# Optimization experiments

Hardware: AMD Instinct MI355X
Metric: run time of the kernel (lower is better)

## Reference

```python
import jax, jax.numpy as jnp
import numpy as np

N, D, B, M, E, Q, MPT = 100000, 128, 512, 4, 10, 5, 8


def setup_inputs() -> dict:
    key = jax.random.key(0)
    ks = jax.random.split(key, 20)
    return {
        "emb": jax.random.normal(ks[0], (N, D), jnp.float32) * 0.05,
        "delta": jax.random.uniform(ks[1], (N,), jnp.float32, 0.5, 1.5),
        "W": jax.random.normal(ks[2], (D, D), jnp.float32) / D,
        "distance_att": jax.random.normal(ks[3], (E,), jnp.float32),
        "metapath_att": jax.random.normal(ks[4], (MPT,), jnp.float32),
        "s_node": jax.random.randint(ks[5], (B,), 0, N, jnp.int32),
        "t_node": jax.random.randint(ks[6], (B,), 0, N, jnp.int32),
        "s_t_time": jax.random.uniform(ks[7], (B,), jnp.float32, 0.0, 10.0),
        "mp_src": jax.random.randint(ks[8], (B, M, E), 0, N, jnp.int32),
        "mp_dst": jax.random.randint(ks[9], (B, M, E), 0, N, jnp.int32),
        "mp_time": jax.random.uniform(ks[10], (B, M, E), jnp.float32, 0.0, 10.0),
        "mp_dist": jax.random.randint(ks[11], (B, M, E), 0, E, jnp.int32),
        "mp_type": jax.random.randint(ks[12], (B, M), 0, MPT, jnp.int32),
        "neg_node": jax.random.randint(ks[13], (B, Q), 0, N, jnp.int32),
        "neg_mp_src": jax.random.randint(ks[14], (B, Q, M, E), 0, N, jnp.int32),
        "neg_mp_dst": jax.random.randint(ks[15], (B, Q, M, E), 0, N, jnp.int32),
        "neg_mp_time": jax.random.uniform(ks[16], (B, Q, M, E), jnp.float32, 0.0, 10.0),
        "neg_mp_dist": jax.random.randint(ks[17], (B, Q, M, E), 0, E, jnp.int32),
        "neg_mp_type": jax.random.randint(ks[18], (B, Q, M), 0, MPT, jnp.int32),
    }


def reference(emb, delta, W, distance_att, metapath_att,
              s_node, t_node, s_t_time,
              mp_src, mp_dst, mp_time, mp_dist, mp_type,
              neg_node, neg_mp_src, neg_mp_dst, neg_mp_time, neg_mp_dist, neg_mp_type):
    eps = 1e-6

    def sim(ea, eb):
        # bilinear similarity e_a^T W e_b, broadcast over leading dims
        return jnp.sum((ea @ W) * eb, axis=-1)

    dis_att = jax.nn.softmax(distance_att)      # [E]
    mp_att = jax.nn.softmax(metapath_att)       # [MPT]

    d_s = delta[s_node]                          # [B]
    d_t = delta[t_node]                          # [B]

    # ---- positive metapath influence ----
    edge_sim = sim(emb[mp_src], emb[mp_dst])                       # [B,M,E]
    decay = jnp.exp(-(d_s * d_t)[:, None, None]
                    * jnp.abs(s_t_time[:, None, None] - mp_time))  # [B,M,E]
    single_mp = jnp.sum(edge_sim * dis_att[mp_dist] * decay, -1)   # [B,M]
    mp_influ = jnp.sum(single_mp * mp_att[mp_type], -1)            # [B]
    p_lambda = sim(emb[s_node], emb[t_node]) + mp_influ            # [B]

    # ---- negative samples ----
    d_neg = delta[neg_node]                                        # [B,Q]
    n_edge_sim = sim(emb[neg_mp_src], emb[neg_mp_dst])             # [B,Q,M,E]
    n_decay = jnp.exp(-(d_s[:, None] * d_neg)[:, :, None, None]
                      * jnp.abs(s_t_time[:, None, None, None] - neg_mp_time))
    n_single = jnp.sum(n_edge_sim * dis_att[neg_mp_dist] * n_decay, -1)  # [B,Q,M]
    n_influ = jnp.sum(n_single * mp_att[neg_mp_type], -1)          # [B,Q]
    s_neg_sim = sim(emb[s_node][:, None, :], emb[neg_node])        # [B,Q]
    n_lambda = jnp.sum(jnp.log(jax.nn.sigmoid(-(s_neg_sim + n_influ)) + eps), -1)  # [B]

    loss = -jnp.log(jax.nn.sigmoid(p_lambda) + eps) - n_lambda     # [B]
    return loss
```

## Files before the change

kernel.cpp:

```cpp
#include <hip/hip_runtime.h>
#include <hip/hip_bf16.h>
#include <math.h>

constexpr int D   = 128;
constexpr int M   = 4;
constexpr int E   = 10;
constexpr int Q   = 5;
constexpr int MPT = 8;
constexpr int MXE = M * E;
constexpr int TASKS = 1 + MXE + Q + Q * MXE;

__global__ __launch_bounds__(256, 4)
void embw_gemm(const float* __restrict__ emb,
               const float* __restrict__ W,
               float* __restrict__ embW,
               int nrows)
{
    const int jg   = threadIdx.x & 15;
    const int rg   = threadIdx.x >> 4;
    const int base = blockIdx.x * 128;
    int row0 = base + rg * 8;
    if (row0 + 8 > nrows) row0 = nrows - 8;

    const float* ap = emb + (size_t)row0 * D;
    const float* wp = W + jg * 4;

    float acc[8][8];
#pragma unroll
    for (int r = 0; r < 8; ++r)
#pragma unroll
        for (int c = 0; c < 8; ++c) acc[r][c] = 0.f;

    float4 a[8];

#pragma unroll 1
    for (int i0 = 0; i0 < D; i0 += 8) {
#pragma unroll
        for (int r = 0; r < 8; ++r)
            a[r] = *reinterpret_cast<const float4*>(ap + r * D + i0);
#pragma unroll
        for (int u = 0; u < 4; ++u) {
            const float4 wlo = *reinterpret_cast<const float4*>(wp + u * D);
            const float4 whi = *reinterpret_cast<const float4*>(wp + u * D + 64);
#pragma unroll
            for (int r = 0; r < 8; ++r) {
                float e = (u == 0) ? a[r].x : (u == 1) ? a[r].y
                        : (u == 2) ? a[r].z : a[r].w;
                acc[r][0] = fmaf(e, wlo.x, acc[r][0]);
                acc[r][1] = fmaf(e, wlo.y, acc[r][1]);
                acc[r][2] = fmaf(e, wlo.z, acc[r][2]);
                acc[r][3] = fmaf(e, wlo.w, acc[r][3]);
                acc[r][4] = fmaf(e, whi.x, acc[r][4]);
                acc[r][5] = fmaf(e, whi.y, acc[r][5]);
                acc[r][6] = fmaf(e, whi.z, acc[r][6]);
                acc[r][7] = fmaf(e, whi.w, acc[r][7]);
            }
        }

#pragma unroll
        for (int r = 0; r < 8; ++r)
            a[r] = *reinterpret_cast<const float4*>(ap + r * D + i0 + 4);
#pragma unroll
        for (int u = 0; u < 4; ++u) {
            const float4 wlo = *reinterpret_cast<const float4*>(wp + (4 + u) * D);
            const float4 whi = *reinterpret_cast<const float4*>(wp + (4 + u) * D + 64);
#pragma unroll
            for (int r = 0; r < 8; ++r) {
                float e = (u == 0) ? a[r].x : (u == 1) ? a[r].y
                        : (u == 2) ? a[r].z : a[r].w;
                acc[r][0] = fmaf(e, wlo.x, acc[r][0]);
                acc[r][1] = fmaf(e, wlo.y, acc[r][1]);
                acc[r][2] = fmaf(e, wlo.z, acc[r][2]);
                acc[r][3] = fmaf(e, wlo.w, acc[r][3]);
                acc[r][4] = fmaf(e, whi.x, acc[r][4]);
                acc[r][5] = fmaf(e, whi.y, acc[r][5]);
                acc[r][6] = fmaf(e, whi.z, acc[r][6]);
                acc[r][7] = fmaf(e, whi.w, acc[r][7]);
            }
        }

        wp += 8 * D;
    }

#pragma unroll
    for (int r = 0; r < 8; ++r) {
        float* rowp = embW + (size_t)(row0 + r) * D;
        *reinterpret_cast<float4*>(rowp + jg * 4) =
            make_float4(acc[r][0], acc[r][1], acc[r][2], acc[r][3]);
        *reinterpret_cast<float4*>(rowp + 64 + jg * 4) =
            make_float4(acc[r][4], acc[r][5], acc[r][6], acc[r][7]);
    }
}

__device__ __forceinline__ void block_softmaxes(const float* distance_att,
                                                const float* metapath_att,
                                                float* s_dis, float* s_mp,
                                                int tid)
{
    if (tid == 0) {
        float v[E];
        float mx = -1e30f;
        for (int i = 0; i < E; ++i) { v[i] = distance_att[i]; mx = fmaxf(mx, v[i]); }
        float sum = 0.f;
        for (int i = 0; i < E; ++i) { v[i] = expf(v[i] - mx); sum += v[i]; }
        for (int i = 0; i < E; ++i) s_dis[i] = v[i] / sum;

        float w[MPT];
        mx = -1e30f;
        for (int i = 0; i < MPT; ++i) { w[i] = metapath_att[i]; mx = fmaxf(mx, w[i]); }
        sum = 0.f;
        for (int i = 0; i < MPT; ++i) { w[i] = expf(w[i] - mx); sum += w[i]; }
        for (int i = 0; i < MPT; ++i) s_mp[i] = w[i] / sum;
    }
}

__device__ __forceinline__ void decode_task(
    int task, int b, int s, int t, float tt, float dss, float dsdt,
    const float* __restrict__ delta,
    const float* __restrict__ s_dis, const float* __restrict__ s_mp,
    const int* __restrict__ mp_src, const int* __restrict__ mp_dst,
    const float* __restrict__ mp_time, const int* __restrict__ mp_dist,
    const int* __restrict__ mp_type,
    const int* __restrict__ neg_node,
    const int* __restrict__ neg_mp_src, const int* __restrict__ neg_mp_dst,
    const float* __restrict__ neg_mp_time, const int* __restrict__ neg_mp_dist,
    const int* __restrict__ neg_mp_type,
    int& srcn, int& dstn, int& slot, float& wgt)
{
    if (task == 0) {
        srcn = s; dstn = t; slot = 0; wgt = 1.f;
    } else if (task <= MXE) {
        int pe = task - 1;
        int m  = pe / E;
        int idx = b * MXE + pe;
        srcn = mp_src[idx];
        dstn = mp_dst[idx];
        slot = 0;
        float dec = expf(-dsdt * fabsf(tt - mp_time[idx]));
        wgt = s_dis[mp_dist[idx]] * dec * s_mp[mp_type[b * M + m]];
    } else if (task <= MXE + Q) {
        int q = task - 1 - MXE;
        srcn = s;
        dstn = neg_node[b * Q + q];
        slot = 1 + q;
        wgt  = 1.f;
    } else {
        int ne  = task - 1 - MXE - Q;
        int q   = ne / MXE;
        int rem = ne - q * MXE;
        int m   = rem / E;
        int idx = (b * Q + q) * MXE + rem;
        srcn = neg_mp_src[idx];
        dstn = neg_mp_dst[idx];
        slot = 1 + q;
        float dneg = delta[neg_node[b * Q + q]];
        float dec  = expf(-(dss * dneg) * fabsf(tt - neg_mp_time[idx]));
        wgt = s_dis[neg_mp_dist[idx]] * dec * s_mp[neg_mp_type[(b * Q + q) * M + m]];
    }
}

__device__ __forceinline__ void epilogue(const float* slots, float* out, int b)
{
    const float eps = 1e-6f;
    float p = slots[0];
    float loss = -logf(1.f / (1.f + expf(-p)) + eps);
#pragma unroll
    for (int q = 0; q < Q; ++q) {
        float v = slots[1 + q];
        loss -= logf(1.f / (1.f + expf(v)) + eps);
    }
    out[b] = loss;
}

__global__ __launch_bounds__(1024)
void pair_kernel(const float* __restrict__ emb,
                 const float* __restrict__ embW,
                 const float* __restrict__ delta,
                 const float* __restrict__ distance_att,
                 const float* __restrict__ metapath_att,
                 const int*   __restrict__ s_node,
                 const int*   __restrict__ t_node,
                 const float* __restrict__ s_t_time,
                 const int*   __restrict__ mp_src,
                 const int*   __restrict__ mp_dst,
                 const float* __restrict__ mp_time,
                 const int*   __restrict__ mp_dist,
                 const int*   __restrict__ mp_type,
                 const int*   __restrict__ neg_node,
                 const int*   __restrict__ neg_mp_src,
                 const int*   __restrict__ neg_mp_dst,
                 const float* __restrict__ neg_mp_time,
                 const int*   __restrict__ neg_mp_dist,
                 const int*   __restrict__ neg_mp_type,
                 float* __restrict__ out)
{
    __shared__ float slots[1 + Q];
    __shared__ float s_dis[E];
    __shared__ float s_mp[MPT];

    const int b   = blockIdx.x;
    const int tid = threadIdx.x;

    if (tid < 1 + Q) slots[tid] = 0.f;
    block_softmaxes(distance_att, metapath_att, s_dis, s_mp, tid);
    __syncthreads();

    const int   s    = s_node[b];
    const int   t    = t_node[b];
    const float tt   = s_t_time[b];
    const float dss  = delta[s];
    const float dsdt = dss * delta[t];

    const int sg = tid >> 4;
    const int ln = tid & 15;

    for (int task = sg; task < TASKS; task += 64) {
        int srcn, dstn, slot;
        float wgt;
        decode_task(task, b, s, t, tt, dss, dsdt, delta, s_dis, s_mp,
                    mp_src, mp_dst, mp_time, mp_dist, mp_type,
                    neg_node, neg_mp_src, neg_mp_dst, neg_mp_time,
                    neg_mp_dist, neg_mp_type, srcn, dstn, slot, wgt);

        const float4* pa = reinterpret_cast<const float4*>(embW + (size_t)srcn * D + ln * 8);
        const float4* pb = reinterpret_cast<const float4*>(emb  + (size_t)dstn * D + ln * 8);
        float4 a0 = pa[0], a1 = pa[1];
        float4 b0 = pb[0], b1 = pb[1];
        float d = a0.x * b0.x + a0.y * b0.y + a0.z * b0.z + a0.w * b0.w
                + a1.x * b1.x + a1.y * b1.y + a1.z * b1.z + a1.w * b1.w;
        d += __shfl_xor(d, 8);
        d += __shfl_xor(d, 4);
        d += __shfl_xor(d, 2);
        d += __shfl_xor(d, 1);
        if (ln == 0) atomicAdd(&slots[slot], d * wgt);
    }
    __syncthreads();

    if (tid == 0) epilogue(slots, out, b);
}

__global__ __launch_bounds__(512)
void pair_direct(const float* __restrict__ emb,
                 const float* __restrict__ W,
                 const float* __restrict__ delta,
                 const float* __restrict__ distance_att,
                 const float* __restrict__ metapath_att,
                 const int*   __restrict__ s_node,
                 const int*   __restrict__ t_node,
                 const float* __restrict__ s_t_time,
                 const int*   __restrict__ mp_src,
                 const int*   __restrict__ mp_dst,
                 const float* __restrict__ mp_time,
                 const int*   __restrict__ mp_dist,
                 const int*   __restrict__ mp_type,
                 const int*   __restrict__ neg_node,
                 const int*   __restrict__ neg_mp_src,
                 const int*   __restrict__ neg_mp_dst,
                 const float* __restrict__ neg_mp_time,
                 const int*   __restrict__ neg_mp_dist,
                 const int*   __restrict__ neg_mp_type,
                 float* __restrict__ out)
{
    __shared__ float slots[1 + Q];
    __shared__ float s_dis[E];
    __shared__ float s_mp[MPT];

    const int b   = blockIdx.x;
    const int tid = threadIdx.x;

    if (tid < 1 + Q) slots[tid] = 0.f;
    block_softmaxes(distance_att, metapath_att, s_dis, s_mp, tid);
    __syncthreads();

    const int   s    = s_node[b];
    const int   t    = t_node[b];
    const float tt   = s_t_time[b];
    const float dss  = delta[s];
    const float dsdt = dss * delta[t];

    const int wave = tid >> 6;
    const int ln   = tid & 63;

    for (int task = wave; task < TASKS; task += 8) {
        int srcn, dstn, slot;
        float wgt;
        decode_task(task, b, s, t, tt, dss, dsdt, delta, s_dis, s_mp,
                    mp_src, mp_dst, mp_time, mp_dist, mp_type,
                    neg_node, neg_mp_src, neg_mp_dst, neg_mp_time,
                    neg_mp_dist, neg_mp_type, srcn, dstn, slot, wgt);

        const float* erow = emb + (size_t)srcn * D;
        float v0 = 0.f, v1 = 0.f;
#pragma unroll 1
        for (int i = 0; i < D; ++i) {
            float a = erow[i];
            v0 = fmaf(a, W[i * D + ln], v0);
            v1 = fmaf(a, W[i * D + ln + 64], v1);
        }
        const float* drow = emb + (size_t)dstn * D;
        float d = v0 * drow[ln] + v1 * drow[ln + 64];
        d += __shfl_xor(d, 32);
        d += __shfl_xor(d, 16);
        d += __shfl_xor(d, 8);
        d += __shfl_xor(d, 4);
        d += __shfl_xor(d, 2);
        d += __shfl_xor(d, 1);
        if (ln == 0) atomicAdd(&slots[slot], d * wgt);
    }
    __syncthreads();

    if (tid == 0) epilogue(slots, out, b);
}

extern "C" void kernel_launch(void* const* d_in, const int* in_sizes, int n_in,
                              void* d_out, int out_size, void* d_ws, size_t ws_size,
                              hipStream_t stream)
{
    const float* emb          = (const float*)d_in[0];
    const float* delta        = (const float*)d_in[1];
    const float* W            = (const float*)d_in[2];
    const float* distance_att = (const float*)d_in[3];
    const float* metapath_att = (const float*)d_in[4];
    const int*   s_node       = (const int*)d_in[5];
    const int*   t_node       = (const int*)d_in[6];
    const float* s_t_time     = (const float*)d_in[7];
    const int*   mp_src       = (const int*)d_in[8];
    const int*   mp_dst       = (const int*)d_in[9];
    const float* mp_time      = (const float*)d_in[10];
    const int*   mp_dist      = (const int*)d_in[11];
    const int*   mp_type      = (const int*)d_in[12];
    const int*   neg_node     = (const int*)d_in[13];
    const int*   neg_mp_src   = (const int*)d_in[14];
    const int*   neg_mp_dst   = (const int*)d_in[15];
    const float* neg_mp_time  = (const float*)d_in[16];
    const int*   neg_mp_dist  = (const int*)d_in[17];
    const int*   neg_mp_type  = (const int*)d_in[18];

    const int N = in_sizes[1];
    const int B = in_sizes[5];

    const size_t need = (size_t)N * D * sizeof(float);

    if (ws_size >= need) {
        float* embW = (float*)d_ws;
        int blocks1 = (N + 127) / 128;
        embw_gemm<<<blocks1, 256, 0, stream>>>(emb, W, embW, N);
        pair_kernel<<<B, 1024, 0, stream>>>(emb, embW, delta,
                                            distance_att, metapath_att,
                                            s_node, t_node, s_t_time,
                                            mp_src, mp_dst, mp_time, mp_dist, mp_type,
                                            neg_node, neg_mp_src, neg_mp_dst,
                                            neg_mp_time, neg_mp_dist, neg_mp_type,
                                            (float*)d_out);
    } else {
        pair_direct<<<B, 512, 0, stream>>>(emb, W, delta,
                                           distance_att, metapath_att,
                                           s_node, t_node, s_t_time,
                                           mp_src, mp_dst, mp_time, mp_dist, mp_type,
                                           neg_node, neg_mp_src, neg_mp_dst,
                                           neg_mp_time, neg_mp_dist, neg_mp_type,
                                           (float*)d_out);
    }
}
```

Baseline: 220.6 us.

## Split embW GEMM into column halves with W staged in shared memory

The emb@W precompute kernel now launches two blocks per 128-row tile, each computing 64 output columns, and stages that half of W in LDS instead of reading it from global memory in the inner loop. Emb row loads are double-buffered so the next float4 chunk loads while the current one is used. This cuts per-thread accumulators and global W traffic, but reads each emb tile twice and adds 32KB of LDS per block, which may limit occupancy.

```diff
diff --git a/kernel.cpp b/kernel.cpp
--- a/kernel.cpp
+++ b/kernel.cpp
@@ -16,79 +16,85 @@
                float* __restrict__ embW,
                int nrows)
 {
-    const int jg   = threadIdx.x & 15;
-    const int rg   = threadIdx.x >> 4;
-    const int base = blockIdx.x * 128;
-    int row0 = base + rg * 8;
+    __shared__ float sW[D * 64];
+
+    const int half    = blockIdx.x & 1;
+    const int tile    = blockIdx.x >> 1;
+    const int colbase = half * 64;
+
+    for (int idx = threadIdx.x; idx < D * 16; idx += 256) {
+        int k  = idx >> 4;
+        int c4 = idx & 15;
+        reinterpret_cast<float4*>(sW)[idx] =
+            *reinterpret_cast<const float4*>(W + (size_t)k * D + colbase + c4 * 4);
+    }
+
+    const int jg = threadIdx.x & 15;
+    const int rg = threadIdx.x >> 4;
+    int row0 = tile * 128 + rg * 8;
     if (row0 + 8 > nrows) row0 = nrows - 8;
 
+    __syncthreads();
+
+    float acc[8][4];
+#pragma unroll
+    for (int r = 0; r < 8; ++r)
+#pragma unroll
+        for (int c = 0; c < 4; ++c) acc[r][c] = 0.f;
+
     const float* ap = emb + (size_t)row0 * D;
-    const float* wp = W + jg * 4;
-
-    float acc[8][8];
+    const float* wb = sW + jg * 4;
+
+    float4 aA[8], aB[8];
 #pragma unroll
     for (int r = 0; r < 8; ++r)
-#pragma unroll
-        for (int c = 0; c < 8; ++c) acc[r][c] = 0.f;
-
-    float4 a[8];
+        aA[r] = *reinterpret_cast<const float4*>(ap + r * D);
 
 #pragma unroll 1
     for (int i0 = 0; i0 < D; i0 += 8) {
 #pragma unroll
         for (int r = 0; r < 8; ++r)
-            a[r] = *reinterpret_cast<const float4*>(ap + r * D + i0);
+            aB[r] = *reinterpret_cast<const float4*>(ap + r * D + i0 + 4);
+
 #pragma unroll
         for (int u = 0; u < 4; ++u) {
-            const float4 wlo = *reinterpret_cast<const float4*>(wp + u * D);
-            const float4 whi = *reinterpret_cast<const float4*>(wp + u * D + 64);
+            const float4 w4 = *reinterpret_cast<const float4*>(&wb[(i0 + u) * 64]);
 #pragma unroll
             for (int r = 0; r < 8; ++r) {
-                float e = (u == 0) ? a[r].x : (u == 1) ? a[r].y
-                        : (u == 2) ? a[r].z : a[r].w;
-                acc[r][0] = fmaf(e, wlo.x, acc[r][0]);
-                acc[r][1] = fmaf(e, wlo.y, acc[r][1]);
-                acc[r][2] = fmaf(e, wlo.z, acc[r][2]);
-                acc[r][3] = fmaf(e, wlo.w, acc[r][3]);
-                acc[r][4] = fmaf(e, whi.x, acc[r][4]);
-                acc[r][5] = fmaf(e, whi.y, acc[r][5]);
-                acc[r][6] = fmaf(e, whi.z, acc[r][6]);
-                acc[r][7] = fmaf(e, whi.w, acc[r][7]);
+                float e = (u == 0) ? aA[r].x : (u == 1) ? aA[r].y
+                        : (u == 2) ? aA[r].z : aA[r].w;
+                acc[r][0] = fmaf(e, w4.x, acc[r][0]);
+                acc[r][1] = fmaf(e, w4.y, acc[r][1]);
+                acc[r][2] = fmaf(e, w4.z, acc[r][2]);
+                acc[r][3] = fmaf(e, w4.w, acc[r][3]);
             }
         }
 
-#pragma unroll
-        for (int r = 0; r < 8; ++r)
-            a[r] = *reinterpret_cast<const float4*>(ap + r * D + i0 + 4);
+        if (i0 + 8 < D) {
+#pragma unroll
+            for (int r = 0; r < 8; ++r)
+                aA[r] = *reinterpret_cast<const float4*>(ap + r * D + i0 + 8);
+        }
+
 #pragma unroll
         for (int u = 0; u < 4; ++u) {
-            const float4 wlo = *reinterpret_cast<const float4*>(wp + (4 + u) * D);
-            const float4 whi = *reinterpret_cast<const float4*>(wp + (4 + u) * D + 64);
+            const float4 w4 = *reinterpret_cast<const float4*>(&wb[(i0 + 4 + u) * 64]);
 #pragma unroll
             for (int r = 0; r < 8; ++r) {
-                float e = (u == 0) ? a[r].x : (u == 1) ? a[r].y
-                        : (u == 2) ? a[r].z : a[r].w;
-                acc[r][0] = fmaf(e, wlo.x, acc[r][0]);
-                acc[r][1] = fmaf(e, wlo.y, acc[r][1]);
-                acc[r][2] = fmaf(e, wlo.z, acc[r][2]);
-                acc[r][3] = fmaf(e, wlo.w, acc[r][3]);
-                acc[r][4] = fmaf(e, whi.x, acc[r][4]);
-                acc[r][5] = fmaf(e, whi.y, acc[r][5]);
-                acc[r][6] = fmaf(e, whi.z, acc[r][6]);
-                acc[r][7] = fmaf(e, whi.w, acc[r][7]);
+                float e = (u == 0) ? aB[r].x : (u == 1) ? aB[r].y
+                        : (u == 2) ? aB[r].z : aB[r].w;
+                acc[r][0] = fmaf(e, w4.x, acc[r][0]);
+                acc[r][1] = fmaf(e, w4.y, acc[r][1]);
+                acc[r][2] = fmaf(e, w4.z, acc[r][2]);
+                acc[r][3] = fmaf(e, w4.w, acc[r][3]);
             }
         }
-
-        wp += 8 * D;
     }
 
 #pragma unroll
     for (int r = 0; r < 8; ++r) {
-        float* rowp = embW + (size_t)(row0 + r) * D;
-        *reinterpret_cast<float4*>(rowp + jg * 4) =
+        *reinterpret_cast<float4*>(embW + (size_t)(row0 + r) * D + colbase + jg * 4) =
             make_float4(acc[r][0], acc[r][1], acc[r][2], acc[r][3]);
-        *reinterpret_cast<float4*>(rowp + 64 + jg * 4) =
-            make_float4(acc[r][4], acc[r][5], acc[r][6], acc[r][7]);
     }
 }
 
@@ -343,8 +349,8 @@
 
     if (ws_size >= need) {
         float* embW = (float*)d_ws;
-        int blocks1 = (N + 127) / 128;
-        embw_gemm<<<blocks1, 256, 0, stream>>>(emb, W, embW, N);
+        int tiles = (N + 127) / 128;
+        embw_gemm<<<tiles * 2, 256, 0, stream>>>(emb, W, embW, N);
         pair_kernel<<<B, 1024, 0, stream>>>(emb, embW, delta,
                                             distance_att, metapath_att,
                                             s_node, t_node, s_t_time,
```

Measured after the change: 392.7 us. +78.0%, slower.
